# Kernel tuning notes

Measured on AMD Instinct MI355X. Metric: run time of the kernel, lower is better.

Reference implementation:

```python
import jax, jax.numpy as jnp
import numpy as np


def setup_inputs() -> dict:
    key = jax.random.key(0)
    ks = jax.random.split(key, 8)
    B, C, D, H, W = 2, 32, 16, 16, 16
    C8 = C // 8
    x = jax.random.normal(ks[0], (B, C, D, H, W), dtype=jnp.float32)
    s = 1.0 / np.sqrt(C)
    wq = jax.random.normal(ks[1], (C8, C), dtype=jnp.float32) * s
    bq = jnp.zeros((C8,), dtype=jnp.float32)
    wk = jax.random.normal(ks[2], (C8, C), dtype=jnp.float32) * s
    bk = jnp.zeros((C8,), dtype=jnp.float32)
    wv = jax.random.normal(ks[3], (C, C), dtype=jnp.float32) * s
    bv = jnp.zeros((C,), dtype=jnp.float32)
    gamma_p = jnp.ones((1,), dtype=jnp.float32)
    gamma_c = jnp.ones((1,), dtype=jnp.float32)
    wo = jax.random.normal(ks[4], (C, 2 * C), dtype=jnp.float32) * (1.0 / np.sqrt(2 * C))
    bo = jnp.zeros((C,), dtype=jnp.float32)
    return {"x": x, "wq": wq, "bq": bq, "wk": wk, "bk": bk,
            "wv": wv, "bv": bv, "gamma_p": gamma_p, "gamma_c": gamma_c,
            "wo": wo, "bo": bo}


def _forward(x, wq, bq, wk, bk, wv, bv, gamma_p, gamma_c, wo, bo):
    B, C, D, H, W = x.shape
    N = D * H * W
    xf = x.reshape(B, C, N)  # [B, C, N]

    # ---- PAM: position attention over N = D*H*W tokens ----
    # 1x1x1 Conv3d == per-token channel matmul
    q = jnp.einsum('oc,bcn->bno', wq, xf) + bq            # [B, N, C/8]
    k = jnp.einsum('oc,bcn->bon', wk, xf) + bk[None, :, None]  # [B, C/8, N]
    v = jnp.einsum('oc,bcn->bon', wv, xf) + bv[None, :, None]  # [B, C, N]
    energy = jnp.einsum('bno,bom->bnm', q, k)             # [B, N, N] (unscaled)
    attn = jax.nn.softmax(energy, axis=-1)                # rows over keys
    # out = v @ attn^T : out[b,c,i] = sum_j v[b,c,j] * attn[b,i,j]
    pam_out = jnp.einsum('bcj,bij->bci', v, attn)         # [B, C, N]
    pam = (gamma_p[0] * pam_out + xf).reshape(B, C, D, H, W)

    # ---- CAM: channel attention with max-subtraction softmax ----
    eng = jnp.einsum('bcn,bdn->bcd', xf, xf)              # [B, C, C]
    eng_new = jnp.max(eng, axis=-1, keepdims=True) - eng
    cattn = jax.nn.softmax(eng_new, axis=-1)              # [B, C, C]
    cam_out = jnp.einsum('bcd,bdn->bcn', cattn, xf)       # [B, C, N]
    cam = (gamma_c[0] * cam_out + xf).reshape(B, C, D, H, W)

    # ---- concat + 1x1x1 out conv ----
    cat = jnp.concatenate([pam, cam], axis=1).reshape(B, 2 * C, N)
    out = jnp.einsum('oc,bcn->bon', wo, cat) + bo[None, :, None]
    return out.reshape(B, C, D, H, W)


def reference(x, wq, bq, wk, bk, wv, bv, gamma_p, gamma_c, wo, bo):
    return _forward(x, wq, bq, wk, bk, wv, bv, gamma_p, gamma_c, wo, bo)
```

## Files before the change

### kernel.cpp

```cpp
#include <hip/hip_runtime.h>
#include <hip/hip_bf16.h>
#include <math.h>

#define BB 2
#define CC 32
#define C8 4
#define NN 4096
#define VST 72
#define LOG2E 1.4426950408889634f

typedef __attribute__((ext_vector_type(8))) short short8;
typedef __attribute__((ext_vector_type(16))) float f32x16;

static __device__ __forceinline__ short f2bf(float x) {
    return __builtin_bit_cast(short, __float2bfloat16(x));
}
static __device__ __forceinline__ unsigned int pkbf(float a, float b) {
    unsigned int ua = __builtin_bit_cast(unsigned int, a) + 0x8000u;
    unsigned int ub = __builtin_bit_cast(unsigned int, b) + 0x8000u;
    return (ua >> 16) | (ub & 0xffff0000u);
}

__global__ __launch_bounds__(256) void k1(const float* __restrict__ x,
    const float* __restrict__ wq, const float* __restrict__ bq,
    const float* __restrict__ wk, const float* __restrict__ bk,
    const float* __restrict__ wv, const float* __restrict__ bv,
    short* __restrict__ qpk, short* __restrict__ kpk, short* __restrict__ vbf,
    float* __restrict__ eng)
{
    if (blockIdx.x >= 64) {
        int w = threadIdx.x >> 6, lane = threadIdx.x & 63;
        int pp = (blockIdx.x - 64)*4 + w;
        int b = pp >= 528 ? 1 : 0;
        int t = pp - b*528;
        int c = 0, rem = t;
        while (rem >= CC - c) { rem -= CC - c; ++c; }
        int d = c + rem;
        const float4* xc = (const float4*)(x + ((size_t)b*CC + c)*NN);
        const float4* xd = (const float4*)(x + ((size_t)b*CC + d)*NN);
        float s = 0.f;
        for (int tt = lane; tt < NN/4; tt += 64) {
            float4 a = xc[tt], bb = xd[tt];
            s += a.x*bb.x + a.y*bb.y + a.z*bb.z + a.w*bb.w;
        }
        #pragma unroll
        for (int off = 32; off; off >>= 1) s += __shfl_down(s, off, 64);
        if (lane == 0) {
            eng[(b*CC + c)*CC + d] = s;
            eng[(b*CC + d)*CC + c] = s;
        }
        return;
    }
    __shared__ float swq[C8*CC], swk[C8*CC], swv[CC*CC], sbq[C8], sbk[C8], sbv[CC];
    int tid = threadIdx.x;
    for (int i = tid; i < C8*CC; i += 256) { swq[i] = wq[i]; swk[i] = wk[i]; }
    for (int i = tid; i < CC*CC; i += 256) swv[i] = wv[i];
    if (tid < C8) { sbq[tid] = bq[tid]; sbk[tid] = bk[tid]; }
    if (tid < CC) sbv[tid] = bv[tid];
    __syncthreads();
    int tl = tid & 127, oh = tid >> 7;
    int g = blockIdx.x*128 + tl;
    int b = g >> 12; int n = g & (NN-1);
    const float* xb = x + (size_t)b*CC*NN + n;
    float xr[CC];
    #pragma unroll
    for (int c = 0; c < CC; ++c) xr[c] = xb[(size_t)c*NN];
    if (oh == 0) {
        float qv[C8], kv[C8];
        #pragma unroll
        for (int o = 0; o < C8; ++o) { qv[o] = sbq[o]; kv[o] = sbk[o]; }
        #pragma unroll
        for (int c = 0; c < CC; ++c) {
            float xc = xr[c];
            #pragma unroll
            for (int o = 0; o < C8; ++o) { qv[o] += swq[o*CC+c]*xc; kv[o] += swk[o*CC+c]*xc; }
        }
        short4 qs = make_short4(f2bf(qv[0]*LOG2E), f2bf(qv[1]*LOG2E),
                                f2bf(qv[2]*LOG2E), f2bf(qv[3]*LOG2E));
        short4 ks = make_short4(f2bf(kv[0]), f2bf(kv[1]), f2bf(kv[2]), f2bf(kv[3]));
        *(short4*)(qpk + ((size_t)b*NN + n)*4) = qs;
        *(short4*)(kpk + ((size_t)b*NN + n)*4) = ks;
    }
    int o0 = oh*16;
    #pragma unroll
    for (int o = 0; o < 16; ++o) {
        float av = sbv[o0+o];
        #pragma unroll
        for (int c = 0; c < CC; ++c) av += swv[(o0+o)*CC+c]*xr[c];
        vbf[((size_t)b*CC+o0+o)*NN + n] = f2bf(av);
    }
}

__global__ __launch_bounds__(1024, 4) void k2(const short* __restrict__ qpk,
    const short* __restrict__ kpk, const short* __restrict__ vbf,
    const float* __restrict__ eng, const float* __restrict__ wo,
    const float* __restrict__ bo, const float* __restrict__ gp,
    const float* __restrict__ gc, const float* __restrict__ x,
    float* __restrict__ out)
{
    __shared__ __align__(16) char smem[99328];

    int blk = blockIdx.x;
    int b  = blk >> 7;
    int it = blk & 127;
    int i0 = it*32;
    int tid = threadIdx.x;
    int w = tid >> 6, lane = tid & 63;
    int qcol = lane & 31, h = lane >> 5;

    short* vbuf = (short*)smem + w*(32*VST);

    int rv = lane >> 1, ch = lane & 1;
    const short* vsrc = vbf + (size_t)b*CC*NN + (size_t)rv*NN + w*64 + ch*32;
    const short* ksrc = kpk + ((size_t)b*NN + w*64 + qcol)*4;

    short8 qf = {0,0,0,0,0,0,0,0};
    if (h == 0) {
        short4 qv = *(const short4*)(qpk + ((size_t)b*NN + i0 + qcol)*4);
        qf[0]=qv.x; qf[1]=qv.y; qf[2]=qv.z; qf[3]=qv.w;
    }

    f32x16 acc = {0,0,0,0,0,0,0,0,0,0,0,0,0,0,0,0};
    const f32x16 zz = {0,0,0,0,0,0,0,0,0,0,0,0,0,0,0,0};
    float se = 0.f;

    short8 cv0 = *(const short8*)(vsrc);
    short8 cv1 = *(const short8*)(vsrc + 8);
    short8 cv2 = *(const short8*)(vsrc + 16);
    short8 cv3 = *(const short8*)(vsrc + 24);
    short4 ck0 = *(const short4*)(ksrc);
    short4 ck1 = *(const short4*)(ksrc + 128);

    #pragma unroll
    for (int t = 0; t < 4; ++t) {
        int tn = t < 3 ? t + 1 : 3;
        short8 nv0 = *(const short8*)(vsrc + tn*1024);
        short8 nv1 = *(const short8*)(vsrc + tn*1024 + 8);
        short8 nv2 = *(const short8*)(vsrc + tn*1024 + 16);
        short8 nv3 = *(const short8*)(vsrc + tn*1024 + 24);
        short4 nk0 = *(const short4*)(ksrc + tn*4096);
        short4 nk1 = *(const short4*)(ksrc + tn*4096 + 128);

        short* wp = vbuf + rv*VST + ch*32;
        *(short8*)(wp)      = cv0;
        *(short8*)(wp + 8)  = cv1;
        *(short8*)(wp + 16) = cv2;
        *(short8*)(wp + 24) = cv3;

        const short* vrow = vbuf + qcol*VST;
        #pragma unroll
        for (int cI = 0; cI < 2; ++cI) {
            short4 kk = cI ? ck1 : ck0;
            short8 kf = {kk.x, kk.y, kk.z, kk.w, 0,0,0,0};
            f32x16 s = __builtin_amdgcn_mfma_f32_32x32x16_bf16(kf, qf, zz, 0, 0, 0);
            float p[16];
            #pragma unroll
            for (int i = 0; i < 16; ++i) p[i] = exp2f(s[i]);
            se += (((p[0]+p[1])+(p[2]+p[3])) + ((p[4]+p[5])+(p[6]+p[7])))
                + (((p[8]+p[9])+(p[10]+p[11])) + ((p[12]+p[13])+(p[14]+p[15])));
            unsigned int u0 = pkbf(p[0],p[1]),   u1 = pkbf(p[2],p[3]);
            unsigned int u2 = pkbf(p[4],p[5]),   u3 = pkbf(p[6],p[7]);
            unsigned int u4 = pkbf(p[8],p[9]),   u5 = pkbf(p[10],p[11]);
            unsigned int u6 = pkbf(p[12],p[13]), u7 = pkbf(p[14],p[15]);
            int vo = cI*32 + 4*h;
            short4 a0 = *(const short4*)(vrow + vo);
            short4 a1 = *(const short4*)(vrow + vo + 8);
            short4 a2 = *(const short4*)(vrow + vo + 16);
            short4 a3 = *(const short4*)(vrow + vo + 24);
            short8 vf1 = {a0.x,a0.y,a0.z,a0.w, a1.x,a1.y,a1.z,a1.w};
            short8 pf1 = {(short)u0,(short)(u0>>16),(short)u1,(short)(u1>>16),
                          (short)u2,(short)(u2>>16),(short)u3,(short)(u3>>16)};
            acc = __builtin_amdgcn_mfma_f32_32x32x16_bf16(vf1, pf1, acc, 0, 0, 0);
            short8 vf2 = {a2.x,a2.y,a2.z,a2.w, a3.x,a3.y,a3.z,a3.w};
            short8 pf2 = {(short)u4,(short)(u4>>16),(short)u5,(short)(u5>>16),
                          (short)u6,(short)(u6>>16),(short)u7,(short)(u7>>16)};
            acc = __builtin_amdgcn_mfma_f32_32x32x16_bf16(vf2, pf2, acc, 0, 0, 0);
        }
        cv0 = nv0; cv1 = nv1; cv2 = nv2; cv3 = nv3;
        ck0 = nk0; ck1 = nk1;
    }

    se += __shfl_xor(se, 32, 64);

    __syncthreads();
    float* pamw = (float*)smem;
    float* seL  = pamw + 16*1056;
    float* sinv = seL  + 512;
    float* pamn = sinv + 32;
    float* xt   = pamn + 1056;
    float* swo  = xt   + 1056;
    float* swx  = swo  + 1056;
    float* sc   = swx  + 1056;
    float* seng = sc   + 1056;
    float* sbo  = seng + 1024;
    float* swo2 = sbo  + 32;

    #pragma unroll
    for (int r = 0; r < 16; ++r) {
        int c = (r&3) + 8*(r>>2) + 4*h;
        pamw[w*1056 + c*33 + qcol] = acc[r];
    }
    if (h == 0) seL[w*32 + qcol] = se;
    for (int i = tid; i < CC*CC; i += 1024) {
        int o = i >> 5, c2 = i & 31;
        seng[i] = eng[b*CC*CC + i];
        swo [o*33 + c2] = wo[o*64 + c2];
        swo2[o*33 + c2] = wo[o*64 + 32 + c2];
        xt  [o*33 + c2] = x[(size_t)b*CC*NN + (size_t)o*NN + i0 + c2];
    }
    if (tid < CC) sbo[tid] = bo[tid];
    __syncthreads();

    if (tid < CC) {
        float s = 0.f;
        #pragma unroll
        for (int w2 = 0; w2 < 16; ++w2) s += seL[w2*32 + tid];
        sinv[tid] = 1.f / s;
    } else if (tid >= 64 && tid < 64 + CC) {
        int r2 = tid - 64;
        float mn = seng[r2*32];
        #pragma unroll
        for (int d = 1; d < CC; ++d) mn = fminf(mn, seng[r2*32 + d]);
        float pv[CC]; float s = 0.f;
        #pragma unroll
        for (int d = 0; d < CC; ++d) { pv[d] = __expf(mn - seng[r2*32 + d]); s += pv[d]; }
        float inv = 1.f / s;
        #pragma unroll
        for (int d = 0; d < CC; ++d) sc[r2*33 + d] = pv[d]*inv;
    }
    __syncthreads();

    float gpv = gp[0], gcv = gc[0];
    for (int i = tid; i < CC*CC; i += 1024) {
        int c = i >> 5, q = i & 31;
        float s2 = 0.f;
        #pragma unroll
        for (int w2 = 0; w2 < 16; ++w2) s2 += pamw[w2*1056 + c*33 + q];
        pamn[c*33 + q] = gpv * s2 * sinv[q];
        float t2 = 0.f;
        #pragma unroll
        for (int c2 = 0; c2 < CC; ++c2) t2 += swo2[c*33 + c2] * sc[c2*33 + q];
        swx[c*33 + q] = swo[c*33 + q] + swo2[c*33 + q] + gcv * t2;
    }
    __syncthreads();

    int q = tid & 31, slot = (tid >> 5) & 31;
    float o0 = sbo[slot];
    #pragma unroll
    for (int c = 0; c < CC; ++c) {
        o0 += swo[slot*33 + c] * pamn[c*33 + q] + swx[slot*33 + c] * xt[c*33 + q];
    }
    out[(size_t)b*CC*NN + (size_t)slot*NN + i0 + q] = o0;
}

extern "C" void kernel_launch(void* const* d_in, const int* in_sizes, int n_in,
                              void* d_out, int out_size, void* d_ws, size_t ws_size,
                              hipStream_t stream)
{
    const float* x  = (const float*)d_in[0];
    const float* wq = (const float*)d_in[1];
    const float* bq = (const float*)d_in[2];
    const float* wk = (const float*)d_in[3];
    const float* bk = (const float*)d_in[4];
    const float* wv = (const float*)d_in[5];
    const float* bv = (const float*)d_in[6];
    const float* gp = (const float*)d_in[7];
    const float* gc = (const float*)d_in[8];
    const float* wo = (const float*)d_in[9];
    const float* bo = (const float*)d_in[10];

    char* wsb = (char*)d_ws;
    short* qpk = (short*)(wsb + 0);
    short* kpk = (short*)(wsb + 65536);
    short* vbf = (short*)(wsb + 131072);
    float* eng = (float*)(wsb + 655360);

    k1<<<328, 256, 0, stream>>>(x, wq, bq, wk, bk, wv, bv, qpk, kpk, vbf, eng);
    k2<<<BB*128, 1024, 0, stream>>>(qpk, kpk, vbf, eng, wo, bo, gp, gc, x, (float*)d_out);
}
```

Before: 28.41 us.

## Shrink LDS and registers: two-phase partial reduction, drop register prefetch

Halves the per-wave PAM partial-sum scratch in shared memory by having waves 8-15 add their accumulators into the slots of waves 0-7 after an extra barrier, cutting LDS from about 97KB to 72KB. The software prefetch of V and K into registers is removed, with loads now issued inline each iteration. The exp/pack loop is restructured into groups of four to shorten register live ranges. The aim is lower LDS and VGPR pressure so more blocks can be resident, at the cost of an extra barrier and less latency hiding for the global loads.

New measurement: 38.04 us. 33.9% more time.

```diff
diff --git a/kernel.cpp b/kernel.cpp
--- a/kernel.cpp
+++ b/kernel.cpp
@@ -98,7 +98,7 @@
     const float* __restrict__ gc, const float* __restrict__ x,
     float* __restrict__ out)
 {
-    __shared__ __align__(16) char smem[99328];
+    __shared__ __align__(16) char smem[73728];
 
     int blk = blockIdx.x;
     int b  = blk >> 7;
@@ -124,67 +124,58 @@
     const f32x16 zz = {0,0,0,0,0,0,0,0,0,0,0,0,0,0,0,0};
     float se = 0.f;
 
-    short8 cv0 = *(const short8*)(vsrc);
-    short8 cv1 = *(const short8*)(vsrc + 8);
-    short8 cv2 = *(const short8*)(vsrc + 16);
-    short8 cv3 = *(const short8*)(vsrc + 24);
-    short4 ck0 = *(const short4*)(ksrc);
-    short4 ck1 = *(const short4*)(ksrc + 128);
-
     #pragma unroll
     for (int t = 0; t < 4; ++t) {
-        int tn = t < 3 ? t + 1 : 3;
-        short8 nv0 = *(const short8*)(vsrc + tn*1024);
-        short8 nv1 = *(const short8*)(vsrc + tn*1024 + 8);
-        short8 nv2 = *(const short8*)(vsrc + tn*1024 + 16);
-        short8 nv3 = *(const short8*)(vsrc + tn*1024 + 24);
-        short4 nk0 = *(const short4*)(ksrc + tn*4096);
-        short4 nk1 = *(const short4*)(ksrc + tn*4096 + 128);
-
-        short* wp = vbuf + rv*VST + ch*32;
-        *(short8*)(wp)      = cv0;
-        *(short8*)(wp + 8)  = cv1;
-        *(short8*)(wp + 16) = cv2;
-        *(short8*)(wp + 24) = cv3;
-
+        {
+            short8 cv0 = *(const short8*)(vsrc + t*1024);
+            short8 cv1 = *(const short8*)(vsrc + t*1024 + 8);
+            short8 cv2 = *(const short8*)(vsrc + t*1024 + 16);
+            short8 cv3 = *(const short8*)(vsrc + t*1024 + 24);
+            short* wp = vbuf + rv*VST + ch*32;
+            *(short8*)(wp)      = cv0;
+            *(short8*)(wp + 8)  = cv1;
+            *(short8*)(wp + 16) = cv2;
+            *(short8*)(wp + 24) = cv3;
+        }
         const short* vrow = vbuf + qcol*VST;
         #pragma unroll
         for (int cI = 0; cI < 2; ++cI) {
-            short4 kk = cI ? ck1 : ck0;
-            short8 kf = {kk.x, kk.y, kk.z, kk.w, 0,0,0,0};
+            short8 kf = {0,0,0,0,0,0,0,0};
+            if (h == 0) {
+                short4 kk = *(const short4*)(ksrc + t*4096 + cI*128);
+                kf[0]=kk.x; kf[1]=kk.y; kf[2]=kk.z; kf[3]=kk.w;
+            }
             f32x16 s = __builtin_amdgcn_mfma_f32_32x32x16_bf16(kf, qf, zz, 0, 0, 0);
-            float p[16];
+            unsigned int u[8];
             #pragma unroll
-            for (int i = 0; i < 16; ++i) p[i] = exp2f(s[i]);
-            se += (((p[0]+p[1])+(p[2]+p[3])) + ((p[4]+p[5])+(p[6]+p[7])))
-                + (((p[8]+p[9])+(p[10]+p[11])) + ((p[12]+p[13])+(p[14]+p[15])));
-            unsigned int u0 = pkbf(p[0],p[1]),   u1 = pkbf(p[2],p[3]);
-            unsigned int u2 = pkbf(p[4],p[5]),   u3 = pkbf(p[6],p[7]);
-            unsigned int u4 = pkbf(p[8],p[9]),   u5 = pkbf(p[10],p[11]);
-            unsigned int u6 = pkbf(p[12],p[13]), u7 = pkbf(p[14],p[15]);
+            for (int g4 = 0; g4 < 4; ++g4) {
+                float p0 = exp2f(s[4*g4]),   p1 = exp2f(s[4*g4+1]);
+                float p2 = exp2f(s[4*g4+2]), p3 = exp2f(s[4*g4+3]);
+                se += (p0+p1)+(p2+p3);
+                u[2*g4]   = pkbf(p0,p1);
+                u[2*g4+1] = pkbf(p2,p3);
+            }
             int vo = cI*32 + 4*h;
             short4 a0 = *(const short4*)(vrow + vo);
             short4 a1 = *(const short4*)(vrow + vo + 8);
+            short8 vf1 = {a0.x,a0.y,a0.z,a0.w, a1.x,a1.y,a1.z,a1.w};
+            short8 pf1 = {(short)u[0],(short)(u[0]>>16),(short)u[1],(short)(u[1]>>16),
+                          (short)u[2],(short)(u[2]>>16),(short)u[3],(short)(u[3]>>16)};
+            acc = __builtin_amdgcn_mfma_f32_32x32x16_bf16(vf1, pf1, acc, 0, 0, 0);
             short4 a2 = *(const short4*)(vrow + vo + 16);
             short4 a3 = *(const short4*)(vrow + vo + 24);
-            short8 vf1 = {a0.x,a0.y,a0.z,a0.w, a1.x,a1.y,a1.z,a1.w};
-            short8 pf1 = {(short)u0,(short)(u0>>16),(short)u1,(short)(u1>>16),
-                          (short)u2,(short)(u2>>16),(short)u3,(short)(u3>>16)};
-            acc = __builtin_amdgcn_mfma_f32_32x32x16_bf16(vf1, pf1, acc, 0, 0, 0);
             short8 vf2 = {a2.x,a2.y,a2.z,a2.w, a3.x,a3.y,a3.z,a3.w};
-            short8 pf2 = {(short)u4,(short)(u4>>16),(short)u5,(short)(u5>>16),
-                          (short)u6,(short)(u6>>16),(short)u7,(short)(u7>>16)};
+            short8 pf2 = {(short)u[4],(short)(u[4]>>16),(short)u[5],(short)(u[5]>>16),
+                          (short)u[6],(short)(u[6]>>16),(short)u[7],(short)(u[7]>>16)};
             acc = __builtin_amdgcn_mfma_f32_32x32x16_bf16(vf2, pf2, acc, 0, 0, 0);
         }
-        cv0 = nv0; cv1 = nv1; cv2 = nv2; cv3 = nv3;
-        ck0 = nk0; ck1 = nk1;
     }
 
     se += __shfl_xor(se, 32, 64);
 
     __syncthreads();
     float* pamw = (float*)smem;
-    float* seL  = pamw + 16*1056;
+    float* seL  = pamw + 8*1056;
     float* sinv = seL  + 512;
     float* pamn = sinv + 32;
     float* xt   = pamn + 1056;
@@ -195,10 +186,12 @@
     float* sbo  = seng + 1024;
     float* swo2 = sbo  + 32;
 
-    #pragma unroll
-    for (int r = 0; r < 16; ++r) {
-        int c = (r&3) + 8*(r>>2) + 4*h;
-        pamw[w*1056 + c*33 + qcol] = acc[r];
+    if (w < 8) {
+        #pragma unroll
+        for (int r = 0; r < 16; ++r) {
+            int c = (r&3) + 8*(r>>2) + 4*h;
+            pamw[w*1056 + c*33 + qcol] = acc[r];
+        }
     }
     if (h == 0) seL[w*32 + qcol] = se;
     for (int i = tid; i < CC*CC; i += 1024) {
@@ -210,6 +203,14 @@
     }
     if (tid < CC) sbo[tid] = bo[tid];
     __syncthreads();
+    if (w >= 8) {
+        #pragma unroll
+        for (int r = 0; r < 16; ++r) {
+            int c = (r&3) + 8*(r>>2) + 4*h;
+            pamw[(w-8)*1056 + c*33 + qcol] += acc[r];
+        }
+    }
+    __syncthreads();
 
     if (tid < CC) {
         float s = 0.f;
@@ -235,7 +236,7 @@
         int c = i >> 5, q = i & 31;
         float s2 = 0.f;
         #pragma unroll
-        for (int w2 = 0; w2 < 16; ++w2) s2 += pamw[w2*1056 + c*33 + q];
+        for (int w2 = 0; w2 < 8; ++w2) s2 += pamw[w2*1056 + c*33 + q];
         pamn[c*33 + q] = gpv * s2 * sinv[q];
         float t2 = 0.f;
         #pragma unroll
```
